# Optimization experiments

Measured on AMD Instinct MI355X. Metric: run time of the kernel, lower is better.

Reference implementation:

```python
import jax, jax.numpy as jnp
import numpy as np

N = 100000
E = 1600000
F = 64
THETA = (0.6, -0.4, 0.3, -0.2, 0.1)  # k = 5 polynomial coefficients


def setup_inputs() -> dict:
    key = jax.random.key(0)
    kx, ke = jax.random.split(key)
    x = jax.random.normal(kx, (N, F), dtype=jnp.float32)
    edge_index = jax.random.randint(ke, (2, E), 0, N, dtype=jnp.int64)
    return {"x": x, "edge_index": edge_index}


def _l_sym_mul(feat, src, dst, deg_inv_sqrt, n):
    # L_sym * feat = feat - D^{-1/2} A D^{-1/2} feat
    src_norm = feat[src] * deg_inv_sqrt[src]            # [E, F] gather + scale
    agg = jax.ops.segment_sum(src_norm, dst, num_segments=n)  # scatter-add to dst
    return feat - deg_inv_sqrt * agg


def reference(x, edge_index):
    src, dst = edge_index[0], edge_index[1]
    n = x.shape[0]
    # in-degree from dst, clamp to >= 1, D^{-1/2} as [N, 1]
    deg = jax.ops.segment_sum(jnp.ones((src.shape[0],), dtype=x.dtype), dst,
                              num_segments=n)
    deg = jnp.maximum(deg, 1.0)[:, None]
    deg_inv_sqrt = deg ** -0.5

    h_acc = THETA[0] * x
    feat = x
    for k in range(1, len(THETA)):
        feat = _l_sym_mul(feat, src, dst, deg_inv_sqrt, n)
        h_acc = h_acc + THETA[k] * feat
    return h_acc
```

## Files before the change

kernel.cpp:

```cpp
#include <hip/hip_runtime.h>


constexpr int kF = 64;
constexpr int BSHIFT = 8;
constexpr int NB = 1 << BSHIFT;
constexpr int TILE = 4096;
constexpr int KMAX = 512;

static __device__ __forceinline__ float bfl(unsigned u) {
    return __uint_as_float(u << 16);
}
static __device__ __forceinline__ float bfh(unsigned u) {
    return __uint_as_float(u & 0xffff0000u);
}
static __device__ __forceinline__ unsigned f2bf(float f) {
    unsigned u = __float_as_uint(f);
    return (u + 0x7fffu + ((u >> 16) & 1u)) >> 16;
}
static __device__ __forceinline__ unsigned pack2(float a, float b) {
    return f2bf(a) | (f2bf(b) << 16);
}

__global__ void k_binA(const int* __restrict__ src, const int* __restrict__ dst,
                       unsigned* __restrict__ pairs, int* __restrict__ gcursor,
                       const float4* __restrict__ x4, uint4* __restrict__ xb4,
                       int n8, int E, int K, int cap) {
    __shared__ int hist[KMAX];
    __shared__ int gb[KMAX];
    const int tid = threadIdx.x;
    const long long tb = (long long)blockIdx.x * TILE;
    const int tcount = (int)min((long long)TILE, (long long)E - tb);

    {
        int per = (n8 + gridDim.x - 1) / (int)gridDim.x;
        int b0 = blockIdx.x * per;
        int b1 = min(b0 + per, n8);
        for (int i = b0 + tid; i < b1; i += 512) {
            float4 a = x4[2 * i];
            float4 b = x4[2 * i + 1];
            uint4 o;
            o.x = pack2(a.x, a.y);
            o.y = pack2(a.z, a.w);
            o.z = pack2(b.x, b.y);
            o.w = pack2(b.z, b.w);
            xb4[i] = o;
        }
    }

    hist[tid] = 0;
    __syncthreads();
    for (int i = tid; i < tcount; i += 512)
        atomicAdd(&hist[dst[tb + i] >> BSHIFT], 1);
    __syncthreads();
    int hv = hist[tid];
    gb[tid] = (tid < K && hv > 0) ? atomicAdd(&gcursor[tid], hv) : 0;
    hist[tid] = 0;
    __syncthreads();
    for (int i = tid; i < tcount; i += 512) {
        int d = dst[tb + i];
        int s = src[tb + i];
        int b = d >> BSHIFT;
        int pos = atomicAdd(&hist[b], 1);
        pairs[(size_t)b * cap + gb[b] + pos] =
            ((unsigned)(d & (NB - 1)) << 23) | (unsigned)s;
    }
}

__global__ void k_binB(const unsigned* __restrict__ pairs, const int* __restrict__ gcursor,
                       int* __restrict__ rp, float* __restrict__ dinv,
                       int2* __restrict__ ecsr, int N, int E, int K, int cap) {
    __shared__ int gsc[KMAX];
    __shared__ int cnt[NB];
    __shared__ int stmp[NB];
    __shared__ int excl[NB];
    __shared__ int cur[NB];
    const int b = blockIdx.x;
    const int tid = threadIdx.x;

    int gv = (tid < K) ? gcursor[tid] : 0;
    gsc[tid] = gv;
    __syncthreads();
    for (int o = 1; o < KMAX; o <<= 1) {
        int t = (tid >= o) ? gsc[tid - o] : 0;
        __syncthreads();
        gsc[tid] += t;
        __syncthreads();
    }
    const int ecnt = gcursor[b];
    const int base = gsc[b] - ecnt;
    const unsigned* bp = pairs + (size_t)b * cap;

    if (tid < NB) cnt[tid] = 0;
    __syncthreads();
    for (int i = tid; i < ecnt; i += 512)
        atomicAdd(&cnt[bp[i] >> 23], 1);
    __syncthreads();
    int v = (tid < NB) ? cnt[tid] : 0;
    if (tid < NB) stmp[tid] = v;
    __syncthreads();
    for (int o = 1; o < NB; o <<= 1) {
        int t = (tid >= o && tid < NB) ? stmp[tid - o] : 0;
        __syncthreads();
        if (tid < NB) stmp[tid] += t;
        __syncthreads();
    }
    if (tid < NB) {
        excl[tid] = stmp[tid] - v;
        cur[tid] = stmp[tid] - v;
    }
    __syncthreads();
    for (int i = tid; i < ecnt; i += 512) {
        unsigned p = bp[i];
        int pos = atomicAdd(&cur[p >> 23], 1);
        ecsr[base + pos].x = (int)(p & 0x7FFFFFu);
    }
    int node = (b << BSHIFT) + tid;
    if (tid < NB && node < N) {
        rp[node] = base + excl[tid];
        dinv[node] = rsqrtf(fmaxf((float)v, 1.0f));
    }
    if (b == K - 1 && tid == 0) rp[N] = E;
}

__global__ void k_wtab(int2* __restrict__ ecsr, const float* __restrict__ dinv, int E) {
    int e = blockIdx.x * blockDim.x + threadIdx.x;
    if (e < E) {
        int2 v = ecsr[e];
        v.y = __float_as_int(dinv[v.x]);
        ecsr[e] = v;
    }
}

template <bool FIRST, bool LAST>
__global__ void k_gather(const int* __restrict__ rp, const int2* __restrict__ ecsr,
                         const unsigned short* __restrict__ featin,
                         const float* __restrict__ xf,
                         const float* __restrict__ dinv,
                         unsigned short* __restrict__ featout,
                         float* __restrict__ h,
                         int n, float th0, float theta) {
    int wid = (blockIdx.x * blockDim.x + threadIdx.x) >> 6;
    int lane = threadIdx.x & 63;
    int half = lane >> 5;
    int r = (lane >> 3) & 3;
    int c = lane & 7;
    int node = wid * 2 + half;
    if (wid * 2 >= n) return;
    bool valid = node < n;
    int beg = valid ? rp[node] : 0;
    int end = valid ? rp[node + 1] : 0;
    int len = end - beg;
    int olen = __shfl_xor(len, 32, 64);
    int mlen = (len > olen) ? len : olen;

    float acc[8] = {0.f, 0.f, 0.f, 0.f, 0.f, 0.f, 0.f, 0.f};
    for (int i = 0; i < mlen; i += 8) {
        int j1 = beg + i + r;
        int j2 = j1 + 4;
        bool ok1 = j1 < end;
        bool ok2 = j2 < end;
        int2 e1 = ecsr[ok1 ? j1 : 0];
        int2 e2 = ecsr[ok2 ? j2 : 0];
        int s1 = e1.x;
        int s2 = e2.x;
        float w1 = ok1 ? __int_as_float(e1.y) : 0.0f;
        float w2 = ok2 ? __int_as_float(e2.y) : 0.0f;
        uint4 ra = *(const uint4*)(featin + ((size_t)s1 << 6) + (c << 3));
        uint4 rb = *(const uint4*)(featin + ((size_t)s2 << 6) + (c << 3));
        acc[0] += w1 * bfl(ra.x);
        acc[1] += w1 * bfh(ra.x);
        acc[2] += w1 * bfl(ra.y);
        acc[3] += w1 * bfh(ra.y);
        acc[4] += w1 * bfl(ra.z);
        acc[5] += w1 * bfh(ra.z);
        acc[6] += w1 * bfl(ra.w);
        acc[7] += w1 * bfh(ra.w);
        acc[0] += w2 * bfl(rb.x);
        acc[1] += w2 * bfh(rb.x);
        acc[2] += w2 * bfl(rb.y);
        acc[3] += w2 * bfh(rb.y);
        acc[4] += w2 * bfl(rb.z);
        acc[5] += w2 * bfh(rb.z);
        acc[6] += w2 * bfl(rb.w);
        acc[7] += w2 * bfh(rb.w);
    }
    #pragma unroll
    for (int m = 8; m <= 16; m <<= 1) {
        #pragma unroll
        for (int i = 0; i < 8; ++i)
            acc[i] += __shfl_xor(acc[i], m, 64);
    }

    if (r == 0 && valid) {
        size_t off = ((size_t)node << 6) + (c << 3);
        float f[8];
        if (FIRST) {
            float4 a = *(const float4*)(xf + off);
            float4 b = *(const float4*)(xf + off + 4);
            f[0] = a.x; f[1] = a.y; f[2] = a.z; f[3] = a.w;
            f[4] = b.x; f[5] = b.y; f[6] = b.z; f[7] = b.w;
        } else {
            uint4 rr = *(const uint4*)(featin + off);
            f[0] = bfl(rr.x); f[1] = bfh(rr.x);
            f[2] = bfl(rr.y); f[3] = bfh(rr.y);
            f[4] = bfl(rr.z); f[5] = bfh(rr.z);
            f[6] = bfl(rr.w); f[7] = bfh(rr.w);
        }
        float di = dinv[node];
        float v[8];
        #pragma unroll
        for (int i = 0; i < 8; ++i) v[i] = f[i] - di * acc[i];
        float4 h0, h1;
        if (FIRST) {
            h0 = make_float4(th0 * f[0] + theta * v[0], th0 * f[1] + theta * v[1],
                             th0 * f[2] + theta * v[2], th0 * f[3] + theta * v[3]);
            h1 = make_float4(th0 * f[4] + theta * v[4], th0 * f[5] + theta * v[5],
                             th0 * f[6] + theta * v[6], th0 * f[7] + theta * v[7]);
        } else {
            h0 = *(const float4*)(h + off);
            h1 = *(const float4*)(h + off + 4);
            h0.x += theta * v[0]; h0.y += theta * v[1];
            h0.z += theta * v[2]; h0.w += theta * v[3];
            h1.x += theta * v[4]; h1.y += theta * v[5];
            h1.z += theta * v[6]; h1.w += theta * v[7];
        }
        *(float4*)(h + off) = h0;
        *(float4*)(h + off + 4) = h1;
        if (!LAST) {
            uint4 o;
            o.x = pack2(v[0], v[1]);
            o.y = pack2(v[2], v[3]);
            o.z = pack2(v[4], v[5]);
            o.w = pack2(v[6], v[7]);
            *(uint4*)(featout + off) = o;
        }
    }
}

extern "C" void kernel_launch(void* const* d_in, const int* in_sizes, int n_in,
                              void* d_out, int out_size, void* d_ws, size_t ws_size,
                              hipStream_t stream) {
    const float* x  = (const float*)d_in[0];
    const int*   ei = (const int*)d_in[1];
    const int N = in_sizes[0] / kF;
    const int E = in_sizes[1] / 2;
    const int* src = ei;
    const int* dst = ei + E;
    float* h = (float*)d_out;

    const int K = (N + NB - 1) >> BSHIFT;
    const int cap = 2 * ((E + K - 1) / K);

    char* ws = (char*)d_ws;
    size_t off = 0;
    auto carve = [&](size_t bytes) {
        void* p = ws + off;
        off = (off + bytes + 511) & ~(size_t)511;
        return p;
    };
    int*            gcursor = (int*)carve((size_t)K * 4);
    int*            rp      = (int*)carve((size_t)(N + 1) * 4);
    float*          dinv    = (float*)carve((size_t)N * 4);
    int2*           ecsr    = (int2*)carve((size_t)E * 8);
    unsigned short* xb      = (unsigned short*)carve((size_t)N * kF * 2);
    unsigned short* featA   = (unsigned short*)carve((size_t)N * kF * 2);
    unsigned short* featB   = (unsigned short*)carve((size_t)N * kF * 2);
    unsigned*       pairs   = (unsigned*)carve((size_t)K * cap * 4);

    const float theta[5] = {0.6f, -0.4f, 0.3f, -0.2f, 0.1f};

    const int n8 = N * kF / 8;
    hipMemsetAsync(gcursor, 0, (size_t)K * 4, stream);
    k_binA<<<(E + TILE - 1) / TILE, 512, 0, stream>>>(src, dst, pairs, gcursor,
                                                      (const float4*)x, (uint4*)xb,
                                                      n8, E, K, cap);
    k_binB<<<K, 512, 0, stream>>>(pairs, gcursor, rp, dinv, ecsr, N, E, K, cap);
    k_wtab<<<(E + 511) / 512, 512, 0, stream>>>(ecsr, dinv, E);

    const int nwaves = (N + 1) / 2;
    const int gblocks = (nwaves + 3) / 4;
    k_gather<true, false><<<gblocks, 256, 0, stream>>>(rp, ecsr, xb, x, dinv, featA, h,
                                                       N, theta[0], theta[1]);
    k_gather<false, false><<<gblocks, 256, 0, stream>>>(rp, ecsr, featA, nullptr, dinv, featB, h,
                                                        N, 0.f, theta[2]);
    k_gather<false, false><<<gblocks, 256, 0, stream>>>(rp, ecsr, featB, nullptr, dinv, featA, h,
                                                        N, 0.f, theta[3]);
    k_gather<false, true><<<gblocks, 256, 0, stream>>>(rp, ecsr, featA, nullptr, dinv, nullptr, h,
                                                       N, 0.f, theta[4]);
}
```

Baseline: 286.0 us.

## Compute degree in binning pass, fold weights into CSR build, defer h accumulation

In-degree is now counted with global atomics during the first binning pass, and a small kernel turns it into D^-1/2. The CSR build can then write each edge's source weight directly, which removes the separate weight-table pass over all edges. The gather kernels no longer read and write the fp32 output each hop. They only store bf16 features into four separate buffers, and one final elementwise kernel combines x and the four hops with theta. The cost is global atomics on degree, an extra memset and kernel launch, more workspace, and a first gather that now reads bf16 x instead of fp32 x.

```diff
diff --git a/kernel.cpp b/kernel.cpp
--- a/kernel.cpp
+++ b/kernel.cpp
@@ -23,6 +23,7 @@
 
 __global__ void k_binA(const int* __restrict__ src, const int* __restrict__ dst,
                        unsigned* __restrict__ pairs, int* __restrict__ gcursor,
+                       int* __restrict__ deg,
                        const float4* __restrict__ x4, uint4* __restrict__ xb4,
                        int n8, int E, int K, int cap) {
     __shared__ int hist[KMAX];
@@ -49,8 +50,11 @@
 
     hist[tid] = 0;
     __syncthreads();
-    for (int i = tid; i < tcount; i += 512)
-        atomicAdd(&hist[dst[tb + i] >> BSHIFT], 1);
+    for (int i = tid; i < tcount; i += 512) {
+        int d = dst[tb + i];
+        atomicAdd(&hist[d >> BSHIFT], 1);
+        atomicAdd(&deg[d], 1);
+    }
     __syncthreads();
     int hv = hist[tid];
     gb[tid] = (tid < K && hv > 0) ? atomicAdd(&gcursor[tid], hv) : 0;
@@ -66,8 +70,13 @@
     }
 }
 
+__global__ void k_dinv(const int* __restrict__ deg, float* __restrict__ dinv, int n) {
+    int i = blockIdx.x * blockDim.x + threadIdx.x;
+    if (i < n) dinv[i] = rsqrtf(fmaxf((float)deg[i], 1.0f));
+}
+
 __global__ void k_binB(const unsigned* __restrict__ pairs, const int* __restrict__ gcursor,
-                       int* __restrict__ rp, float* __restrict__ dinv,
+                       const float* __restrict__ dinv, int* __restrict__ rp,
                        int2* __restrict__ ecsr, int N, int E, int K, int cap) {
     __shared__ int gsc[KMAX];
     __shared__ int cnt[NB];
@@ -111,34 +120,19 @@
     __syncthreads();
     for (int i = tid; i < ecnt; i += 512) {
         unsigned p = bp[i];
+        int s = (int)(p & 0x7FFFFFu);
         int pos = atomicAdd(&cur[p >> 23], 1);
-        ecsr[base + pos].x = (int)(p & 0x7FFFFFu);
+        ecsr[base + pos] = make_int2(s, __float_as_int(dinv[s]));
     }
     int node = (b << BSHIFT) + tid;
-    if (tid < NB && node < N) {
-        rp[node] = base + excl[tid];
-        dinv[node] = rsqrtf(fmaxf((float)v, 1.0f));
-    }
+    if (tid < NB && node < N) rp[node] = base + excl[tid];
     if (b == K - 1 && tid == 0) rp[N] = E;
 }
 
-__global__ void k_wtab(int2* __restrict__ ecsr, const float* __restrict__ dinv, int E) {
-    int e = blockIdx.x * blockDim.x + threadIdx.x;
-    if (e < E) {
-        int2 v = ecsr[e];
-        v.y = __float_as_int(dinv[v.x]);
-        ecsr[e] = v;
-    }
-}
-
-template <bool FIRST, bool LAST>
 __global__ void k_gather(const int* __restrict__ rp, const int2* __restrict__ ecsr,
                          const unsigned short* __restrict__ featin,
-                         const float* __restrict__ xf,
                          const float* __restrict__ dinv,
-                         unsigned short* __restrict__ featout,
-                         float* __restrict__ h,
-                         int n, float th0, float theta) {
+                         unsigned short* __restrict__ featout, int n) {
     int wid = (blockIdx.x * blockDim.x + threadIdx.x) >> 6;
     int lane = threadIdx.x & 63;
     int half = lane >> 5;
@@ -193,48 +187,37 @@
 
     if (r == 0 && valid) {
         size_t off = ((size_t)node << 6) + (c << 3);
-        float f[8];
-        if (FIRST) {
-            float4 a = *(const float4*)(xf + off);
-            float4 b = *(const float4*)(xf + off + 4);
-            f[0] = a.x; f[1] = a.y; f[2] = a.z; f[3] = a.w;
-            f[4] = b.x; f[5] = b.y; f[6] = b.z; f[7] = b.w;
-        } else {
-            uint4 rr = *(const uint4*)(featin + off);
-            f[0] = bfl(rr.x); f[1] = bfh(rr.x);
-            f[2] = bfl(rr.y); f[3] = bfh(rr.y);
-            f[4] = bfl(rr.z); f[5] = bfh(rr.z);
-            f[6] = bfl(rr.w); f[7] = bfh(rr.w);
-        }
+        uint4 rr = *(const uint4*)(featin + off);
         float di = dinv[node];
-        float v[8];
-        #pragma unroll
-        for (int i = 0; i < 8; ++i) v[i] = f[i] - di * acc[i];
-        float4 h0, h1;
-        if (FIRST) {
-            h0 = make_float4(th0 * f[0] + theta * v[0], th0 * f[1] + theta * v[1],
-                             th0 * f[2] + theta * v[2], th0 * f[3] + theta * v[3]);
-            h1 = make_float4(th0 * f[4] + theta * v[4], th0 * f[5] + theta * v[5],
-                             th0 * f[6] + theta * v[6], th0 * f[7] + theta * v[7]);
-        } else {
-            h0 = *(const float4*)(h + off);
-            h1 = *(const float4*)(h + off + 4);
-            h0.x += theta * v[0]; h0.y += theta * v[1];
-            h0.z += theta * v[2]; h0.w += theta * v[3];
-            h1.x += theta * v[4]; h1.y += theta * v[5];
-            h1.z += theta * v[6]; h1.w += theta * v[7];
-        }
-        *(float4*)(h + off) = h0;
-        *(float4*)(h + off + 4) = h1;
-        if (!LAST) {
-            uint4 o;
-            o.x = pack2(v[0], v[1]);
-            o.y = pack2(v[2], v[3]);
-            o.z = pack2(v[4], v[5]);
-            o.w = pack2(v[6], v[7]);
-            *(uint4*)(featout + off) = o;
-        }
-    }
+        uint4 o;
+        o.x = pack2(bfl(rr.x) - di * acc[0], bfh(rr.x) - di * acc[1]);
+        o.y = pack2(bfl(rr.y) - di * acc[2], bfh(rr.y) - di * acc[3]);
+        o.z = pack2(bfl(rr.z) - di * acc[4], bfh(rr.z) - di * acc[5]);
+        o.w = pack2(bfl(rr.w) - di * acc[6], bfh(rr.w) - di * acc[7]);
+        *(uint4*)(featout + off) = o;
+    }
+}
+
+__global__ void k_final(const float4* __restrict__ x4,
+                        const uint4* __restrict__ f1, const uint4* __restrict__ f2,
+                        const uint4* __restrict__ f3, const uint4* __restrict__ f4,
+                        float4* __restrict__ h4, int n8,
+                        float t0, float t1, float t2, float t3, float t4) {
+    int i = blockIdx.x * blockDim.x + threadIdx.x;
+    if (i >= n8) return;
+    uint4 a = f1[i], b = f2[i], cc = f3[i], d = f4[i];
+    float4 xa = x4[2 * i], xb = x4[2 * i + 1];
+    float4 h0, h1;
+    h0.x = t0 * xa.x + t1 * bfl(a.x) + t2 * bfl(b.x) + t3 * bfl(cc.x) + t4 * bfl(d.x);
+    h0.y = t0 * xa.y + t1 * bfh(a.x) + t2 * bfh(b.x) + t3 * bfh(cc.x) + t4 * bfh(d.x);
+    h0.z = t0 * xa.z + t1 * bfl(a.y) + t2 * bfl(b.y) + t3 * bfl(cc.y) + t4 * bfl(d.y);
+    h0.w = t0 * xa.w + t1 * bfh(a.y) + t2 * bfh(b.y) + t3 * bfh(cc.y) + t4 * bfh(d.y);
+    h1.x = t0 * xb.x + t1 * bfl(a.z) + t2 * bfl(b.z) + t3 * bfl(cc.z) + t4 * bfl(d.z);
+    h1.y = t0 * xb.y + t1 * bfh(a.z) + t2 * bfh(b.z) + t3 * bfh(cc.z) + t4 * bfh(d.z);
+    h1.z = t0 * xb.z + t1 * bfl(a.w) + t2 * bfl(b.w) + t3 * bfl(cc.w) + t4 * bfl(d.w);
+    h1.w = t0 * xb.w + t1 * bfh(a.w) + t2 * bfh(b.w) + t3 * bfh(cc.w) + t4 * bfh(d.w);
+    h4[2 * i] = h0;
+    h4[2 * i + 1] = h1;
 }
 
 extern "C" void kernel_launch(void* const* d_in, const int* in_sizes, int n_in,
@@ -259,32 +242,39 @@
         return p;
     };
     int*            gcursor = (int*)carve((size_t)K * 4);
+    int*            deg     = (int*)carve((size_t)N * 4);
     int*            rp      = (int*)carve((size_t)(N + 1) * 4);
     float*          dinv    = (float*)carve((size_t)N * 4);
     int2*           ecsr    = (int2*)carve((size_t)E * 8);
     unsigned short* xb      = (unsigned short*)carve((size_t)N * kF * 2);
-    unsigned short* featA   = (unsigned short*)carve((size_t)N * kF * 2);
-    unsigned short* featB   = (unsigned short*)carve((size_t)N * kF * 2);
+    unsigned short* f1      = (unsigned short*)carve((size_t)N * kF * 2);
+    unsigned short* f2      = (unsigned short*)carve((size_t)N * kF * 2);
+    unsigned short* f3      = (unsigned short*)carve((size_t)N * kF * 2);
+    unsigned short* f4      = (unsigned short*)carve((size_t)N * kF * 2);
     unsigned*       pairs   = (unsigned*)carve((size_t)K * cap * 4);
 
     const float theta[5] = {0.6f, -0.4f, 0.3f, -0.2f, 0.1f};
-
     const int n8 = N * kF / 8;
+
     hipMemsetAsync(gcursor, 0, (size_t)K * 4, stream);
-    k_binA<<<(E + TILE - 1) / TILE, 512, 0, stream>>>(src, dst, pairs, gcursor,
+    hipMemsetAsync(deg, 0, (size_t)N * 4, stream);
+    k_binA<<<(E + TILE - 1) / TILE, 512, 0, stream>>>(src, dst, pairs, gcursor, deg,
                                                       (const float4*)x, (uint4*)xb,
                                                       n8, E, K, cap);
-    k_binB<<<K, 512, 0, stream>>>(pairs, gcursor, rp, dinv, ecsr, N, E, K, cap);
-    k_wtab<<<(E + 511) / 512, 512, 0, stream>>>(ecsr, dinv, E);
+    k_dinv<<<(N + 511) / 512, 512, 0, stream>>>(deg, dinv, N);
+    k_binB<<<K, 512, 0, stream>>>(pairs, gcursor, dinv, rp, ecsr, N, E, K, cap);
 
     const int nwaves = (N + 1) / 2;
     const int gblocks = (nwaves + 3) / 4;
-    k_gather<true, false><<<gblocks, 256, 0, stream>>>(rp, ecsr, xb, x, dinv, featA, h,
-                                                       N, theta[0], theta[1]);
-    k_gather<false, false><<<gblocks, 256, 0, stream>>>(rp, ecsr, featA, nullptr, dinv, featB, h,
-                                                        N, 0.f, theta[2]);
-    k_gather<false, false><<<gblocks, 256, 0, stream>>>(rp, ecsr, featB, nullptr, dinv, featA, h,
-                                                        N, 0.f, theta[3]);
-    k_gather<false, true><<<gblocks, 256, 0, stream>>>(rp, ecsr, featA, nullptr, dinv, nullptr, h,
-                                                       N, 0.f, theta[4]);
-}
+    k_gather<<<gblocks, 256, 0, stream>>>(rp, ecsr, xb, dinv, f1, N);
+    k_gather<<<gblocks, 256, 0, stream>>>(rp, ecsr, f1, dinv, f2, N);
+    k_gather<<<gblocks, 256, 0, stream>>>(rp, ecsr, f2, dinv, f3, N);
+    k_gather<<<gblocks, 256, 0, stream>>>(rp, ecsr, f3, dinv, f4, N);
+
+    k_final<<<(n8 + 255) / 256, 256, 0, stream>>>((const float4*)x,
+                                                  (const uint4*)f1, (const uint4*)f2,
+                                                  (const uint4*)f3, (const uint4*)f4,
+                                                  (float4*)h, n8,
+                                                  theta[0], theta[1], theta[2],
+                                                  theta[3], theta[4]);
+}
```

After: 329.7 us. 15.3% more time.
